# Optimization experiments

Hardware: AMD Instinct MI355X
Metric: run time of the kernel (lower is better)

The kernel has to match this reference:

```python
import jax, jax.numpy as jnp
import numpy as np
from jax import lax

EPS = 1e-5  # BatchNorm eps (inference mode)

def _bn(x, g, b, m, v):
    # inference batchnorm over channel axis 1 of NCHW
    s = g / jnp.sqrt(v + EPS)
    return x * s[None, :, None, None] + (b - m * s)[None, :, None, None]

def _conv1x1(w, x):
    # w: [O, C], x: [B, C, H, W]
    return jnp.einsum('oc,bchw->bohw', w, x)

def setup_inputs() -> dict:
    key = jax.random.key(0)
    ks = jax.random.split(key, 40)
    B, Cin, S = 8, 2048, 64
    R, D, H, NC = 128, 512, 64, 19
    f32 = jnp.float32
    def n(k, shape, scale):
        return jax.random.normal(k, shape, dtype=f32) * scale
    inp = {}
    inp['x'] = jax.random.normal(ks[0], (B, Cin, S, S), f32)
    inp['feat_w'] = n(ks[1], (D, Cin, 3, 3), 0.02)
    # 4 batchnorms: feat, encoding, fusion, conv6
    for i, name in enumerate(['bn1', 'bn2', 'bn3', 'bn4']):
        kk = jax.random.split(ks[2 + i], 4)
        inp[name + '_g'] = jax.random.uniform(kk[0], (D,), f32, 0.5, 1.5)
        inp[name + '_b'] = n(kk[1], (D,), 0.05)
        inp[name + '_m'] = n(kk[2], (D,), 0.1)
        inp[name + '_v'] = jax.random.uniform(kk[3], (D,), f32, 0.5, 1.5)
    inp['enc_w'] = n(ks[6], (D, D), 0.05)
    inp['fc_w'] = n(ks[7], (D, D), 0.05)
    inp['fc_b'] = n(ks[8], (D,), 0.05)
    inp['w1'] = n(ks[9], (R, D, D), 0.05)   # conv1_1[i]: 512->512 1x1
    inp['w2'] = n(ks[10], (R, H, H), 0.05)  # conv1_2[i]: 64->64 1x1
    inp['w3'] = n(ks[11], (R, H, H), 0.05)  # conv1_3[i]: 64->64 1x1
    inp['fusion_w'] = n(ks[12], (D, D), 0.05)
    inp['c6a_w'] = n(ks[13], (D, 2 * D), 0.05)
    inp['c6b_w'] = n(ks[14], (NC, D), 0.05)
    inp['c6b_b'] = n(ks[15], (NC,), 0.05)
    return inp

def reference(x, feat_w,
              bn1_g, bn1_b, bn1_m, bn1_v,
              bn2_g, bn2_b, bn2_m, bn2_v,
              bn3_g, bn3_b, bn3_m, bn3_v,
              bn4_g, bn4_b, bn4_m, bn4_v,
              enc_w, fc_w, fc_b, w1, w2, w3,
              fusion_w, c6a_w, c6b_w, c6b_b):
    # self.feat: 3x3 conv -> BN -> ReLU
    feat = jax.nn.relu(_bn(
        lax.conv_general_dilated(x, feat_w, (1, 1), 'SAME',
                                 dimension_numbers=('NCHW', 'OIHW', 'NCHW')),
        bn1_g, bn1_b, bn1_m, bn1_v))

    # EncModule (se_loss=False)
    enc = jax.nn.relu(_bn(_conv1x1(enc_w, feat), bn2_g, bn2_b, bn2_m, bn2_v))
    en = enc.mean(axis=(2, 3))                                # [B, 512]
    gamma = jax.nn.sigmoid(en @ fc_w.T + fc_b)                # [B, 512]
    se_out = jax.nn.relu(feat * (1.0 + gamma[:, :, None, None]))

    # ContextDecomp: pooled mode vectors (AdaptiveAvgPool2d(1) of permutes)
    Cvec = feat.mean(axis=(2, 3))   # [B, 512] channel vector
    Hvec = feat.mean(axis=(1, 2))   # [B, 64]  (avg over channel & height -> width axis)
    Wvec = feat.mean(axis=(1, 3))   # [B, 64]  (avg over channel & width  -> height axis)
    # all 128 rank-wise 1x1 convs + sigmoid, batched over rank r
    CC = jax.nn.sigmoid(jnp.einsum('roc,bc->bro', w1, Cvec))  # [B, R, 512]
    HH = jax.nn.sigmoid(jnp.einsum('roh,bh->bro', w2, Hvec))  # [B, R, 64]
    WW = jax.nn.sigmoid(jnp.einsum('row,bw->bro', w3, Wvec))  # [B, R, 64]
    # Tucker/CP reconstruction summed over ranks; torch layout puts the
    # width-derived vector (HH) on spatial axis 2 and height-derived (WW) on axis 3
    t1 = jnp.einsum('brc,bri,brj->bcij', CC, HH, WW) * 0.015625  # 1/64
    t = feat * (1.0 + t1)
    outs = jax.nn.relu(_bn(_conv1x1(fusion_w, t), bn3_g, bn3_b, bn3_m, bn3_v))

    # conv6 head: cat -> 1x1 conv -> BN -> ReLU -> (dropout eval=id) -> 1x1 conv
    cat = jnp.concatenate([outs, se_out], axis=1)              # [B, 1024, 64, 64]
    h6 = jax.nn.relu(_bn(_conv1x1(c6a_w, cat), bn4_g, bn4_b, bn4_m, bn4_v))
    out = _conv1x1(c6b_w, h6) + c6b_b[None, :, None, None]     # [B, 19, 64, 64]
    return out
```

## Files before the change

kernel.cpp:

```cpp
#include <hip/hip_runtime.h>
#include <stdint.h>
#include <stddef.h>

using u16 = unsigned short;
using u32 = unsigned int;

typedef __attribute__((ext_vector_type(8))) short short8;
typedef __attribute__((ext_vector_type(4))) float f32x4;

#define DEV static __device__ __forceinline__

DEV float bf2f(u16 v){ union{u32 u; float f;} x; x.u = ((u32)v)<<16; return x.f; }
DEV u16 f2bf(float f){ union{float f; u32 u;} x; x.f = f; u32 r = (x.u + 0x7FFFu + ((x.u>>16)&1u))>>16; return (u16)r; }
DEV float lo16(u32 u){ union{u32 u; float f;} x; x.u = u<<16; return x.f; }
DEV float hi16(u32 u){ union{u32 u; float f;} x; x.u = u & 0xFFFF0000u; return x.f; }

DEV void gload16(const u16* g, u16* l){
  __builtin_amdgcn_global_load_lds((const __attribute__((address_space(1))) void*)g,
                                   (__attribute__((address_space(3))) void*)l, 16, 0, 0);
}

#define BAR    __builtin_amdgcn_s_barrier()
#define SCHED0 __builtin_amdgcn_sched_barrier(0)
#define PRIO1  __builtin_amdgcn_s_setprio(1)
#define PRIO0  __builtin_amdgcn_s_setprio(0)
#define VMC4   asm volatile("s_waitcnt vmcnt(4)" ::: "memory")
#define VMC0   asm volatile("s_waitcnt vmcnt(0)" ::: "memory")

__global__ __launch_bounds__(512, 2)
void conv_gemm256(const u16* __restrict__ xp, const u16* __restrict__ wt,
                  u16* __restrict__ O, const float* __restrict__ sb,
                  float* __restrict__ Cvec, float* __restrict__ Hvec,
                  float* __restrict__ Wvec)
{
  constexpr int NT = 288;
  __shared__ u16 smA[2*256*64];
  __shared__ u16 smB[2*256*64];
  const int t = threadIdx.x;
  const int lane = t & 63;
  const int wv = t >> 6;
  const int wr = wv >> 2, wc = wv & 3;
  const int mt = blockIdx.x, nt = blockIdx.y, b = blockIdx.z;
  const int ij0 = mt*256, n0 = nt*256;
  const u16* Ab = xp + (size_t)b*66*66*2048;

  const int tA   = t >> 3;
  const int sc8  = ((t&7) ^ ((t>>3)&7)) * 8;
  const int ldsc = (t&7) * 8;
  const int qB   = t >> 8;
  const int rB   = (t>>3) & 31;

  f32x4 acc[8][4];
  #pragma unroll
  for (int i=0;i<8;++i)
    #pragma unroll
    for (int j=0;j<4;++j) acc[i][j] = (f32x4){0.f,0.f,0.f,0.f};

  short8 aR[4][2];
  short8 bR[2][2][2];

#define STG_A(dst, s, kt_) do{ \
    const int ktc = (kt_) < NT ? (kt_) : (NT-1); \
    const int tap = ktc>>5; const int ty = (tap*11)>>5; const int tx = tap - ty*3; \
    const size_t ko = ((size_t)(ktc&31))<<6; \
    _Pragma("unroll") for (int l=0;l<2;++l){ \
      const int row = (s)*64 + tA + l*128; \
      const u16* src = Ab + ((size_t)((mt*4 + (s) + l*2 + ty)*66 + tA + tx))*2048 + ko + sc8; \
      gload16(src, (dst) + row*64 + ldsc); } }while(0)

#define STG_B(dst, s, kt_) do{ \
    const int ktc = (kt_) < NT ? (kt_) : (NT-1); \
    const int tap = ktc>>5; \
    const size_t ko = (size_t)tap*2048 + (((size_t)(ktc&31))<<6); \
    _Pragma("unroll") for (int l=0;l<2;++l){ \
      const int row = (l*2 + qB)*64 + (s)*32 + rB; \
      const u16* src = wt + ((size_t)(n0 + row))*9*2048 + ko + sc8; \
      gload16(src, (dst) + row*64 + ldsc); } }while(0)

#define LDA_(base, mh) do{ _Pragma("unroll") for(int mi=0;mi<4;++mi){ \
    const int r = wr*128 + (mh)*64 + mi*16 + (lane&15); \
    _Pragma("unroll") for(int kk=0;kk<2;++kk){ \
      const int ch = (kk*4 + (lane>>4)) ^ (r&7); \
      aR[mi][kk] = *(const short8*)&(base)[r*64 + ch*8]; } } }while(0)
#define LDB_(base, nh) do{ _Pragma("unroll") for(int ni=0;ni<2;++ni){ \
    const int r = wc*64 + (nh)*32 + ni*16 + (lane&15); \
    _Pragma("unroll") for(int kk=0;kk<2;++kk){ \
      const int ch = (kk*4 + (lane>>4)) ^ (r&7); \
      bR[nh][ni][kk] = *(const short8*)&(base)[r*64 + ch*8]; } } }while(0)
#define MFMAQ(mh, nh) do{ _Pragma("unroll") for(int mi=0;mi<4;++mi) \
    _Pragma("unroll") for(int ni=0;ni<2;++ni){ \
      acc[(mh)*4+mi][(nh)*2+ni] = __builtin_amdgcn_mfma_f32_16x16x32_bf16(aR[mi][0], bR[nh][ni][0], acc[(mh)*4+mi][(nh)*2+ni],0,0,0); \
      acc[(mh)*4+mi][(nh)*2+ni] = __builtin_amdgcn_mfma_f32_16x16x32_bf16(aR[mi][1], bR[nh][ni][1], acc[(mh)*4+mi][(nh)*2+ni],0,0,0); } }while(0)

  STG_A(smA, 0, 0);
  STG_B(smB, 0, 0);
  STG_B(smB, 1, 0);
  STG_A(smA, 1, 0);
  VMC4;
  BAR; SCHED0;

  for (int j=0; j<NT; ++j) {
    const int p = j & 1;
    const u16* As = smA + (p<<14);
    const u16* Bs = smB + (p<<14);
    u16* Aalt = smA + ((p^1)<<14);
    u16* Balt = smB + ((p^1)<<14);

    LDA_(As, 0); LDB_(Bs, 0);
    STG_A(Aalt, 0, j+1);
    BAR; SCHED0;
    PRIO1; MFMAQ(0,0); PRIO0;
    VMC4;
    BAR; SCHED0;

    LDB_(Bs, 1);
    STG_B(Balt, 0, j+1);
    BAR; SCHED0;
    PRIO1; MFMAQ(0,1); PRIO0;
    VMC4;
    BAR; SCHED0;

    LDA_(As, 1);
    STG_B(Balt, 1, j+1);
    BAR; SCHED0;
    PRIO1; MFMAQ(1,0); PRIO0;
    BAR; SCHED0;

    STG_A(Aalt, 1, j+1);
    BAR; SCHED0;
    PRIO1; MFMAQ(1,1); PRIO0;
    VMC4;
    BAR; SCHED0;
  }

  VMC0;
  BAR;
  float* red = (float*)smA;
  if (t < 324) red[t] = 0.f;
  BAR;

  float xs[4][4];
  #pragma unroll
  for (int q=0;q<4;++q)
    #pragma unroll
    for (int j2=0;j2<4;++j2) xs[q][j2] = 0.f;
  float ys0 = 0.f, ys1 = 0.f;

  #pragma unroll
  for (int n=0; n<4; ++n) {
    const int cloc = wc*64 + (n>>1)*32 + (n&1)*16 + (lane&15);
    const int col = n0 + cloc;
    const float s = sb[col], bb = sb[512+col];
    float cs = 0.f;
    #pragma unroll
    for (int a=0; a<8; ++a) {
      const int row0 = ij0 + wr*128 + (a>>2)*64 + (a&3)*16 + ((lane>>4)<<2);
      #pragma unroll
      for (int j2=0; j2<4; ++j2) {
        const size_t idx = ((size_t)(b*4096 + row0 + j2))*512 + col;
        float v = acc[a][n][j2]*s + bb;
        v = v > 0.f ? v : 0.f;
        O[idx] = f2bf(v);
        cs += v;
        xs[a&3][j2] += v;
        if (a < 4) ys0 += v; else ys1 += v;
      }
    }
    atomicAdd(&red[cloc], cs);
  }
  #pragma unroll
  for (int off=1; off<16; off<<=1)
    #pragma unroll
    for (int q=0;q<4;++q)
      #pragma unroll
      for (int j2=0;j2<4;++j2) xs[q][j2] += __shfl_xor(xs[q][j2], off);
  if ((lane & 15) == 0) {
    #pragma unroll
    for (int q=0;q<4;++q)
      #pragma unroll
      for (int j2=0;j2<4;++j2)
        atomicAdd(&red[256 + q*16 + (lane>>4)*4 + j2], xs[q][j2]);
  }
  #pragma unroll
  for (int off=1; off<64; off<<=1) { ys0 += __shfl_xor(ys0, off); ys1 += __shfl_xor(ys1, off); }
  if (lane == 0) {
    atomicAdd(&red[320 + wr*2 + 0], ys0);
    atomicAdd(&red[320 + wr*2 + 1], ys1);
  }
  BAR;
  if (t < 256)       atomicAdd(&Cvec[b*512 + n0 + t], red[t]*(1.0f/4096.0f));
  else if (t < 320)  atomicAdd(&Hvec[b*64 + (t-256)], red[t]*(1.0f/32768.0f));
  else if (t < 324)  atomicAdd(&Wvec[b*64 + (ij0>>6) + (t-320)], red[t]*(1.0f/32768.0f));
#undef STG_A
#undef STG_B
#undef LDA_
#undef LDB_
#undef MFMAQ
}

template<int V>
__global__ __launch_bounds__(512, 2)
void gemm256(const u16* __restrict__ A0, const u16* __restrict__ A1,
             const u16* __restrict__ Bw0, const u16* __restrict__ Bw1,
             u16* __restrict__ O, const float* __restrict__ sb,
             float* __restrict__ en)
{
  constexpr int NTALL = (V==4) ? 16 : 8;
  __shared__ u16 smA[2*256*64];
  __shared__ u16 smB[2*256*64];
  const int t = threadIdx.x;
  const int lane = t & 63;
  const int wv = t >> 6;
  const int wr = wv >> 2, wc = wv & 3;
  const int mt = blockIdx.x, nt = blockIdx.y, b = blockIdx.z;
  const int ij0 = mt*256, n0 = nt*256;
  const u16* A0b = A0 + (size_t)b*4096*512;
  const u16* A1b = (V==4) ? (A1 + (size_t)b*4096*512) : nullptr;
  const u16* B1b = (V==4) ? (Bw1 + (size_t)b*512*512) : nullptr;

  const int tA   = t >> 3;
  const int sc8  = ((t&7) ^ ((t>>3)&7)) * 8;
  const int ldsc = (t&7) * 8;
  const int qB   = t >> 8;
  const int rB   = (t>>3) & 31;

  f32x4 acc[8][4];
  #pragma unroll
  for (int i=0;i<8;++i)
    #pragma unroll
    for (int j=0;j<4;++j) acc[i][j] = (f32x4){0.f,0.f,0.f,0.f};

  short8 aR[4][2];
  short8 bR[2][2][2];

#define STG_A(dst, s, kt_) do{ \
    const int ktc = (kt_) < NTALL ? (kt_) : (NTALL-1); \
    const u16* Abase = (V==4 && ktc>=8) ? A1b : A0b; \
    const size_t ko = ((size_t)(ktc&7))<<6; \
    _Pragma("unroll") for (int l=0;l<2;++l){ \
      const int row = (s)*64 + tA + l*128; \
      const u16* src = Abase + (size_t)(ij0 + row)*512 + ko + sc8; \
      gload16(src, (dst) + row*64 + ldsc); } }while(0)

#define STG_B(dst, s, kt_) do{ \
    const int ktc = (kt_) < NTALL ? (kt_) : (NTALL-1); \
    const u16* Bbase = (V==4 && ktc>=8) ? B1b : Bw0; \
    const size_t ko = ((size_t)(ktc&7))<<6; \
    _Pragma("unroll") for (int l=0;l<2;++l){ \
      const int row = (l*2 + qB)*64 + (s)*32 + rB; \
      const u16* src = Bbase + (size_t)(n0 + row)*512 + ko + sc8; \
      gload16(src, (dst) + row*64 + ldsc); } }while(0)

#define LDA_(base, mh) do{ _Pragma("unroll") for(int mi=0;mi<4;++mi){ \
    const int r = wr*128 + (mh)*64 + mi*16 + (lane&15); \
    _Pragma("unroll") for(int kk=0;kk<2;++kk){ \
      const int ch = (kk*4 + (lane>>4)) ^ (r&7); \
      aR[mi][kk] = *(const short8*)&(base)[r*64 + ch*8]; } } }while(0)
#define LDB_(base, nh) do{ _Pragma("unroll") for(int ni=0;ni<2;++ni){ \
    const int r = wc*64 + (nh)*32 + ni*16 + (lane&15); \
    _Pragma("unroll") for(int kk=0;kk<2;++kk){ \
      const int ch = (kk*4 + (lane>>4)) ^ (r&7); \
      bR[nh][ni][kk] = *(const short8*)&(base)[r*64 + ch*8]; } } }while(0)
#define MFMAQ(mh, nh) do{ _Pragma("unroll") for(int mi=0;mi<4;++mi) \
    _Pragma("unroll") for(int ni=0;ni<2;++ni){ \
      acc[(mh)*4+mi][(nh)*2+ni] = __builtin_amdgcn_mfma_f32_16x16x32_bf16(aR[mi][0], bR[nh][ni][0], acc[(mh)*4+mi][(nh)*2+ni],0,0,0); \
      acc[(mh)*4+mi][(nh)*2+ni] = __builtin_amdgcn_mfma_f32_16x16x32_bf16(aR[mi][1], bR[nh][ni][1], acc[(mh)*4+mi][(nh)*2+ni],0,0,0); } }while(0)

  STG_A(smA, 0, 0);
  STG_B(smB, 0, 0);
  STG_B(smB, 1, 0);
  STG_A(smA, 1, 0);
  VMC4;
  BAR; SCHED0;

  for (int j=0; j<NTALL; ++j) {
    const int p = j & 1;
    const u16* As = smA + (p<<14);
    const u16* Bs = smB + (p<<14);
    u16* Aalt = smA + ((p^1)<<14);
    u16* Balt = smB + ((p^1)<<14);

    LDA_(As, 0); LDB_(Bs, 0);
    STG_A(Aalt, 0, j+1);
    BAR; SCHED0;
    PRIO1; MFMAQ(0,0); PRIO0;
    VMC4;
    BAR; SCHED0;

    LDB_(Bs, 1);
    STG_B(Balt, 0, j+1);
    BAR; SCHED0;
    PRIO1; MFMAQ(0,1); PRIO0;
    VMC4;
    BAR; SCHED0;

    LDA_(As, 1);
    STG_B(Balt, 1, j+1);
    BAR; SCHED0;
    PRIO1; MFMAQ(1,0); PRIO0;
    BAR; SCHED0;

    STG_A(Aalt, 1, j+1);
    BAR; SCHED0;
    PRIO1; MFMAQ(1,1); PRIO0;
    VMC4;
    BAR; SCHED0;
  }
  VMC0;

  if constexpr (V==1) {
    #pragma unroll
    for (int n=0; n<4; ++n) {
      const int col = n0 + wc*64 + (n>>1)*32 + (n&1)*16 + (lane&15);
      const float s = sb[col], bb = sb[512+col];
      float cs = 0.f;
      #pragma unroll
      for (int a=0; a<8; ++a) {
        #pragma unroll
        for (int j2=0; j2<4; ++j2) {
          float v = acc[a][n][j2]*s + bb;
          cs += (v > 0.f) ? v : 0.f;
        }
      }
      cs += __shfl_xor(cs, 16);
      cs += __shfl_xor(cs, 32);
      if (lane < 16) atomicAdd(&en[b*512 + col], cs * (1.0f/4096.0f));
    }
  } else {
    #pragma unroll
    for (int n=0; n<4; ++n) {
      const int col = n0 + wc*64 + (n>>1)*32 + (n&1)*16 + (lane&15);
      const float s = sb[col], bb = sb[512+col];
      #pragma unroll
      for (int a=0; a<8; ++a) {
        const int row0 = ij0 + wr*128 + (a>>2)*64 + (a&3)*16 + ((lane>>4)<<2);
        #pragma unroll
        for (int j2=0; j2<4; ++j2) {
          const size_t idx = ((size_t)(b*4096 + row0 + j2))*512 + col;
          float v = acc[a][n][j2]*s + bb;
          O[idx] = f2bf(v > 0.f ? v : 0.f);
        }
      }
    }
  }
#undef STG_A
#undef STG_B
#undef LDA_
#undef LDB_
#undef MFMAQ
}

template<int V>
__global__ __launch_bounds__(256)
void gemm128(const u16* __restrict__ A, const u16* __restrict__ Bw, u16* __restrict__ O,
             const u16* __restrict__ feat, const u16* __restrict__ B2,
             const float* __restrict__ sb, float* __restrict__ en)
{
  constexpr int KSEG = 128;
  __shared__ u16 smA[128*64];
  __shared__ u16 smB[128*64];
  const int tid = threadIdx.x;
  const int lane = tid & 63;
  const int wv = tid >> 6;
  const int wr = wv >> 1, wc = wv & 1;
  const int mt = blockIdx.x, nt = blockIdx.y, b = blockIdx.z;
  const int ij0 = mt*128, n0 = nt*128;
  const int srow = tid >> 3, schunk = tid & 7;

  f32x4 acc[4][4];
  #pragma unroll
  for (int i=0;i<4;++i)
    #pragma unroll
    for (int j=0;j<4;++j) acc[i][j] = (f32x4){0.f,0.f,0.f,0.f};

  const u16* Ab = A + (size_t)b*4096*128;
  const u16* Bb = Bw + (size_t)b*512*128;

  for (int kt=0; kt<KSEG/64; ++kt) {
    const int k0 = kt*64;
    #pragma unroll
    for (int i=0;i<4;++i) {
      const int row = i*32 + srow;
      const int sc = schunk ^ (row & 7);
      gload16(Ab + (size_t)(ij0+row)*128 + (k0 + sc*8), &smA[row*64 + schunk*8]);
    }
    #pragma unroll
    for (int i=0;i<4;++i) {
      const int row = i*32 + srow;
      const int sc = schunk ^ (row & 7);
      gload16(Bb + (size_t)(n0+row)*128 + (k0 + sc*8), &smB[row*64 + schunk*8]);
    }
    __syncthreads();
    #pragma unroll
    for (int ks=0; ks<2; ++ks) {
      short8 av[4], bv[4];
      #pragma unroll
      for (int mi=0;mi<4;++mi) {
        const int r = wr*64 + mi*16 + (lane & 15);
        const int ch = (ks*4 + (lane>>4)) ^ (r & 7);
        av[mi] = *(const short8*)&smA[r*64 + ch*8];
      }
      #pragma unroll
      for (int ni=0;ni<4;++ni) {
        const int r = wc*64 + ni*16 + (lane & 15);
        const int ch = (ks*4 + (lane>>4)) ^ (r & 7);
        bv[ni] = *(const short8*)&smB[r*64 + ch*8];
      }
      #pragma unroll
      for (int mi=0;mi<4;++mi)
        #pragma unroll
        for (int ni=0;ni<4;++ni)
          acc[mi][ni] = __builtin_amdgcn_mfma_f32_16x16x32_bf16(av[mi], bv[ni], acc[mi][ni], 0, 0, 0);
    }
    __syncthreads();
  }

  #pragma unroll
  for (int ni=0;ni<4;++ni) {
    const int col = n0 + wc*64 + ni*16 + (lane & 15);
    #pragma unroll
    for (int mi=0;mi<4;++mi) {
      const int row0 = ij0 + wr*64 + mi*16 + ((lane>>4)<<2);
      #pragma unroll
      for (int j=0;j<4;++j) {
        const size_t idx = ((size_t)(b*4096 + row0 + j))*512 + col;
        O[idx] = f2bf(bf2f(feat[idx]) * (1.0f + acc[mi][ni][j]));
      }
    }
  }
}

__global__ __launch_bounds__(256)
void prep_weights(const float* __restrict__ fw, const float* __restrict__ encw,
                  const float* __restrict__ fusw, const float* __restrict__ c6aw,
                  const float* g1,const float* b1,const float* m1,const float* v1,
                  const float* g2,const float* b2,const float* m2,const float* v2,
                  const float* g3,const float* b3,const float* m3,const float* v3,
                  const float* g4,const float* b4,const float* m4,const float* v4,
                  u16* __restrict__ wt, u16* __restrict__ encb,
                  u16* __restrict__ fusb, u16* __restrict__ c6a1,
                  float* __restrict__ bnsb)
{
  const int bx = blockIdx.x, t = threadIdx.x;
  if (bx < 512) {
    const int o = bx;
    for (int c = t; c < 2048; c += 256) {
      const float* src = fw + ((size_t)o*2048 + c)*9;
      #pragma unroll
      for (int tt=0; tt<9; ++tt)
        wt[((size_t)o*9 + tt)*2048 + c] = f2bf(src[tt]);
    }
  } else if (bx < 1536) {
    const int i = (bx-512)*256 + t;
    encb[i] = f2bf(encw[i]);
  } else if (bx < 2560) {
    const int i = (bx-1536)*256 + t;
    fusb[i] = f2bf(fusw[i]);
  } else if (bx < 3584) {
    const int i = (bx-2560)*256 + t;
    c6a1[i] = f2bf(c6aw[(size_t)(i>>9)*1024 + (i&511)]);
  } else {
    const int c = (bx-3584)*256 + t;
    if (c < 512) {
      const float eps = 1e-5f;
      float s1 = g1[c]*rsqrtf(v1[c]+eps); bnsb[c]      = s1; bnsb[512+c]  = b1[c]-m1[c]*s1;
      float s2 = g2[c]*rsqrtf(v2[c]+eps); bnsb[1024+c] = s2; bnsb[1536+c] = b2[c]-m2[c]*s2;
      float s3 = g3[c]*rsqrtf(v3[c]+eps); bnsb[2048+c] = s3; bnsb[2560+c] = b3[c]-m3[c]*s3;
      float s4 = g4[c]*rsqrtf(v4[c]+eps); bnsb[3072+c] = s4; bnsb[3584+c] = b4[c]-m4[c]*s4;
    }
  }
}

__global__ __launch_bounds__(256)
void pad_x(const float* __restrict__ x, u16* __restrict__ xp)
{
  __shared__ u16 tile[256*66];
  const int bx = blockIdx.x;
  const int cb = bx & 7, y = (bx>>3) & 63, b = bx >> 9;
  const int t = threadIdx.x;
  const int xcol = t & 63, crow = t >> 6;
  for (int it=0; it<64; ++it) {
    const int cl = it*4 + crow;
    tile[cl*66 + xcol] = f2bf(x[(((size_t)b*2048 + cb*256 + cl)*64 + y)*64 + xcol]);
  }
  __syncthreads();
  const size_t rowbase = (size_t)(b*66 + y + 1)*66;
  for (int px=0; px<64; ++px)
    xp[(rowbase + px + 1)*2048 + cb*256 + t] = tile[t*66 + px];
  xp[rowbase*2048 + cb*256 + t] = 0;
  xp[(rowbase + 65)*2048 + cb*256 + t] = 0;
  if (y == 0) {
    const size_t rb = (size_t)(b*66)*66;
    for (int px=0; px<66; ++px) xp[(rb+px)*2048 + cb*256 + t] = 0;
  }
  if (y == 63) {
    const size_t rb = (size_t)(b*66 + 65)*66;
    for (int px=0; px<66; ++px) xp[(rb+px)*2048 + cb*256 + t] = 0;
  }
}

__global__ __launch_bounds__(256)
void small1(const float* __restrict__ en, const float* __restrict__ fcw, const float* __restrict__ fcb,
            const float* __restrict__ w1, const float* __restrict__ Cvec,
            const float* __restrict__ w2, const float* __restrict__ w3,
            const float* __restrict__ Hvec, const float* __restrict__ Wvec,
            float* __restrict__ gamma, u16* __restrict__ CCT,
            float* __restrict__ HH, float* __restrict__ WW)
{
  const int bx = blockIdx.x, t = threadIdx.x;
  if (bx < 8) {
    __shared__ float enl[512];
    const int b = bx;
    for (int c=t;c<512;c+=256) enl[c] = en[b*512+c];
    __syncthreads();
    for (int o=t;o<512;o+=256) {
      float a = fcb[o];
      const float* wr = fcw + (size_t)o*512;
      for (int c=0;c<512;++c) a += enl[c]*wr[c];
      gamma[b*512+o] = 1.0f/(1.0f+__expf(-a));
    }
  } else if (bx < 136) {
    __shared__ float hl[512], wl[512];
    const int r = bx - 8;
    for (int i=t;i<512;i+=256){ hl[i]=Hvec[i]; wl[i]=Wvec[i]; }
    __syncthreads();
    const int i = t & 63, bh = t >> 6;
    for (int bb=bh; bb<8; bb+=4) {
      float sh=0.f, sw=0.f;
      const float* w2r = w2 + ((size_t)r*64 + i)*64;
      const float* w3r = w3 + ((size_t)r*64 + i)*64;
      #pragma unroll 8
      for (int h=0;h<64;++h){ sh += w2r[h]*hl[bb*64+h]; sw += w3r[h]*wl[bb*64+h]; }
      HH[((size_t)bb*128 + r)*64 + i] = 1.0f/(1.0f+__expf(-sh));
      WW[((size_t)bb*128 + r)*64 + i] = 1.0f/(1.0f+__expf(-sw));
    }
  } else {
    __shared__ float cv[4096];
    for (int i=t;i<4096;i+=256) cv[i] = Cvec[i];
    __syncthreads();
    const int p = (bx-136)*4 + (t>>6);
    const int r = p >> 9, o = p & 511;
    const int lane = t & 63;
    float ab[8] = {0,0,0,0,0,0,0,0};
    const float* w1r = w1 + ((size_t)r*512 + o)*512;
    #pragma unroll
    for (int it=0; it<8; ++it) {
      const float wvv = w1r[it*64 + lane];
      #pragma unroll
      for (int bb=0;bb<8;++bb) ab[bb] += wvv * cv[bb*512 + it*64 + lane];
    }
    #pragma unroll
    for (int off=32; off; off>>=1)
      #pragma unroll
      for (int bb=0;bb<8;++bb) ab[bb] += __shfl_xor(ab[bb], off);
    #pragma unroll
    for (int bb=0;bb<8;++bb)
      if (lane == bb)
        CCT[((size_t)bb*512 + o)*128 + r] = f2bf((1.0f/(1.0f+__expf(-ab[bb]))) * 0.015625f);
  }
}

__global__ __launch_bounds__(256)
void small2(const float* __restrict__ c6aw, const float* __restrict__ gamma,
            const float* __restrict__ HH, const float* __restrict__ WW,
            u16* __restrict__ w2b, u16* __restrict__ HWT)
{
  const int bx = blockIdx.x, t = threadIdx.x;
  if (bx < 4096) {
    const int b = bx >> 9, o = bx & 511;
    const float* src = c6aw + (size_t)o*1024 + 512;
    const float* gmv = gamma + b*512;
    u16* dst = w2b + ((size_t)b*512 + o)*512;
    for (int c=t;c<512;c+=256) dst[c] = f2bf(src[c]*(1.0f+gmv[c]));
  } else {
    __shared__ float wwl[64*129];
    __shared__ float hhy[128];
    const int idx = bx - 4096;
    const int b = idx >> 6, y = idx & 63;
    for (int g=t; g<8192; g+=256){ const int r=g>>6, xx=g&63; wwl[xx*129+r] = WW[((size_t)b*128+r)*64+xx]; }
    if (t < 128) hhy[t] = HH[((size_t)b*128 + t)*64 + y];
    __syncthreads();
    const int r2 = (t & 63)*2, xg = t >> 6;
    for (int xx=xg; xx<64; xx+=4) {
      const float v0 = hhy[r2]   * wwl[xx*129 + r2];
      const float v1 = hhy[r2+1] * wwl[xx*129 + r2 + 1];
      const u32 pk = (u32)f2bf(v0) | ((u32)f2bf(v1)<<16);
      *(u32*)&HWT[((size_t)(b*4096 + y*64 + xx))*128 + r2] = pk;
    }
  }
}

__global__ __launch_bounds__(256)
void c6b_head(const u16* __restrict__ h6, const float* __restrict__ w,
              const float* __restrict__ bias, float* __restrict__ out)
{
  const int gid = blockIdx.x*256 + threadIdx.x;
  const int b = gid >> 12, ij = gid & 4095;
  float acc[19];
  #pragma unroll
  for (int o=0;o<19;++o) acc[o] = bias[o];
  const u16* hp = h6 + (size_t)gid*512;
  for (int c0=0;c0<512;c0+=8) {
    const uint4 d = *(const uint4*)(hp + c0);
    const float f0=lo16(d.x),f1=hi16(d.x),f2=lo16(d.y),f3=hi16(d.y),
                f4=lo16(d.z),f5=hi16(d.z),f6=lo16(d.w),f7=hi16(d.w);
    #pragma unroll
    for (int o=0;o<19;++o) {
      const float* wr = w + o*512 + c0;
      acc[o] += f0*wr[0] + f1*wr[1] + f2*wr[2] + f3*wr[3]
              + f4*wr[4] + f5*wr[5] + f6*wr[6] + f7*wr[7];
    }
  }
  #pragma unroll
  for (int o=0;o<19;++o) out[((size_t)(b*19 + o))*4096 + ij] = acc[o];
}

extern "C" void kernel_launch(void* const* d_in, const int* in_sizes, int n_in,
                              void* d_out, int out_size, void* d_ws, size_t ws_size,
                              hipStream_t stream)
{
  (void)in_sizes; (void)n_in; (void)out_size;
  const float* x     = (const float*)d_in[0];
  const float* fw    = (const float*)d_in[1];
  const float* bnp[16];
  for (int i=0;i<16;++i) bnp[i] = (const float*)d_in[2+i];
  const float* enc_w = (const float*)d_in[18];
  const float* fc_w  = (const float*)d_in[19];
  const float* fc_b  = (const float*)d_in[20];
  const float* w1    = (const float*)d_in[21];
  const float* w2    = (const float*)d_in[22];
  const float* w3    = (const float*)d_in[23];
  const float* fus_w = (const float*)d_in[24];
  const float* c6a_w = (const float*)d_in[25];
  const float* c6b_w = (const float*)d_in[26];
  const float* c6b_b = (const float*)d_in[27];

  char* ws = (char*)d_ws;
  constexpr size_t OFF_XP=0, OFF_T=0, OFF_OUTS=33554432ull, OFF_H6=67108864ull,
    OFF_WT=142737408ull, OFF_FEAT=161611776ull, OFF_HWT=195166208ull, OFF_W2B=203554816ull,
    OFF_CCT=207749120ull, OFF_ENCB=208797696ull, OFF_FUSB=209321984ull, OFF_C6A1=209846272ull,
    OFF_HH=210370560ull, OFF_WW=210632704ull, OFF_EN=210894848ull, OFF_CV=210911232ull,
    OFF_HV=210927616ull, OFF_WV=210929664ull, OFF_GAMMA=210931712ull, OFF_BNSB=210948096ull,
    NEEDED=210964480ull;
  if (ws_size < NEEDED) return;

  u16* xp    = (u16*)(ws + OFF_XP);
  u16* tb    = (u16*)(ws + OFF_T);
  u16* outs  = (u16*)(ws + OFF_OUTS);
  u16* h6    = (u16*)(ws + OFF_H6);
  u16* wt    = (u16*)(ws + OFF_WT);
  u16* featb = (u16*)(ws + OFF_FEAT);
  u16* hwt   = (u16*)(ws + OFF_HWT);
  u16* w2b   = (u16*)(ws + OFF_W2B);
  u16* cct   = (u16*)(ws + OFF_CCT);
  u16* encb  = (u16*)(ws + OFF_ENCB);
  u16* fusb  = (u16*)(ws + OFF_FUSB);
  u16* c6a1  = (u16*)(ws + OFF_C6A1);
  float* HH  = (float*)(ws + OFF_HH);
  float* WW  = (float*)(ws + OFF_WW);
  float* en  = (float*)(ws + OFF_EN);
  float* Cv  = (float*)(ws + OFF_CV);
  float* Hv  = (float*)(ws + OFF_HV);
  float* Wv  = (float*)(ws + OFF_WV);
  float* gm  = (float*)(ws + OFF_GAMMA);
  float* bnsb= (float*)(ws + OFF_BNSB);

  hipMemsetAsync(ws + OFF_EN, 0, 36864, stream);

  prep_weights<<<3586,256,0,stream>>>(fw, enc_w, fus_w, c6a_w,
      bnp[0],bnp[1],bnp[2],bnp[3], bnp[4],bnp[5],bnp[6],bnp[7],
      bnp[8],bnp[9],bnp[10],bnp[11], bnp[12],bnp[13],bnp[14],bnp[15],
      wt, encb, fusb, c6a1, bnsb);
  pad_x<<<4096,256,0,stream>>>(x, xp);
  conv_gemm256<<<dim3(16,2,8),512,0,stream>>>(xp, wt, featb, bnsb, Cv, Hv, Wv);
  gemm256<1><<<dim3(16,2,8),512,0,stream>>>(featb, nullptr, encb, nullptr, nullptr, bnsb+1024, en);
  small1<<<16520,256,0,stream>>>(en, fc_w, fc_b, w1, Cv, w2, w3, Hv, Wv, gm, cct, HH, WW);
  small2<<<4608,256,0,stream>>>(c6a_w, gm, HH, WW, w2b, hwt);
  gemm128<2><<<dim3(32,4,8),256,0,stream>>>(hwt, cct, tb, featb, nullptr, nullptr, nullptr);
  gemm256<3><<<dim3(16,2,8),512,0,stream>>>(tb, nullptr, fusb, nullptr, outs, bnsb+2048, nullptr);
  gemm256<4><<<dim3(16,2,8),512,0,stream>>>(outs, featb, c6a1, w2b, h6, bnsb+3072, nullptr);
  c6b_head<<<128,256,0,stream>>>(h6, c6b_w, c6b_b, (float*)d_out);
}
```

Baseline: 953.7 us.

## Restructure conv GEMM main loop with single-barrier schedule and vectorize helper kernels

```diff
diff --git a/kernel.cpp b/kernel.cpp
--- a/kernel.cpp
+++ b/kernel.cpp
@@ -4,6 +4,7 @@
 
 using u16 = unsigned short;
 using u32 = unsigned int;
+using u64 = unsigned long long;
 
 typedef __attribute__((ext_vector_type(8))) short short8;
 typedef __attribute__((ext_vector_type(4))) float f32x4;
@@ -26,8 +27,9 @@
 #define PRIO0  __builtin_amdgcn_s_setprio(0)
 #define VMC4   asm volatile("s_waitcnt vmcnt(4)" ::: "memory")
 #define VMC0   asm volatile("s_waitcnt vmcnt(0)" ::: "memory")
-
-__global__ __launch_bounds__(512, 2)
+#define SGB(m,n) __builtin_amdgcn_sched_group_barrier((m),(n),0)
+
+__global__ __launch_bounds__(512, 1)
 void conv_gemm256(const u16* __restrict__ xp, const u16* __restrict__ wt,
                   u16* __restrict__ O, const float* __restrict__ sb,
                   float* __restrict__ Cvec, float* __restrict__ Hvec,
@@ -56,7 +58,7 @@
     #pragma unroll
     for (int j=0;j<4;++j) acc[i][j] = (f32x4){0.f,0.f,0.f,0.f};
 
-  short8 aR[4][2];
+  short8 aR[2][4][2];
   short8 bR[2][2][2];
 
 #define STG_A(dst, s, kt_) do{ \
@@ -81,7 +83,7 @@
     const int r = wr*128 + (mh)*64 + mi*16 + (lane&15); \
     _Pragma("unroll") for(int kk=0;kk<2;++kk){ \
       const int ch = (kk*4 + (lane>>4)) ^ (r&7); \
-      aR[mi][kk] = *(const short8*)&(base)[r*64 + ch*8]; } } }while(0)
+      aR[mh][mi][kk] = *(const short8*)&(base)[r*64 + ch*8]; } } }while(0)
 #define LDB_(base, nh) do{ _Pragma("unroll") for(int ni=0;ni<2;++ni){ \
     const int r = wc*64 + (nh)*32 + ni*16 + (lane&15); \
     _Pragma("unroll") for(int kk=0;kk<2;++kk){ \
@@ -89,15 +91,15 @@
       bR[nh][ni][kk] = *(const short8*)&(base)[r*64 + ch*8]; } } }while(0)
 #define MFMAQ(mh, nh) do{ _Pragma("unroll") for(int mi=0;mi<4;++mi) \
     _Pragma("unroll") for(int ni=0;ni<2;++ni){ \
-      acc[(mh)*4+mi][(nh)*2+ni] = __builtin_amdgcn_mfma_f32_16x16x32_bf16(aR[mi][0], bR[nh][ni][0], acc[(mh)*4+mi][(nh)*2+ni],0,0,0); \
-      acc[(mh)*4+mi][(nh)*2+ni] = __builtin_amdgcn_mfma_f32_16x16x32_bf16(aR[mi][1], bR[nh][ni][1], acc[(mh)*4+mi][(nh)*2+ni],0,0,0); } }while(0)
+      acc[(mh)*4+mi][(nh)*2+ni] = __builtin_amdgcn_mfma_f32_16x16x32_bf16(aR[mh][mi][0], bR[nh][ni][0], acc[(mh)*4+mi][(nh)*2+ni],0,0,0); \
+      acc[(mh)*4+mi][(nh)*2+ni] = __builtin_amdgcn_mfma_f32_16x16x32_bf16(aR[mh][mi][1], bR[nh][ni][1], acc[(mh)*4+mi][(nh)*2+ni],0,0,0); } }while(0)
 
   STG_A(smA, 0, 0);
   STG_B(smB, 0, 0);
   STG_B(smB, 1, 0);
   STG_A(smA, 1, 0);
-  VMC4;
-  BAR; SCHED0;
+  VMC0;
+  BAR;
 
   for (int j=0; j<NT; ++j) {
     const int p = j & 1;
@@ -106,35 +108,33 @@
     u16* Aalt = smA + ((p^1)<<14);
     u16* Balt = smB + ((p^1)<<14);
 
+    STG_A(Aalt, 0, j+1);
+    STG_B(Balt, 0, j+1);
+    STG_B(Balt, 1, j+1);
+    STG_A(Aalt, 1, j+1);
+
     LDA_(As, 0); LDB_(Bs, 0);
-    STG_A(Aalt, 0, j+1);
-    BAR; SCHED0;
-    PRIO1; MFMAQ(0,0); PRIO0;
-    VMC4;
-    BAR; SCHED0;
-
-    LDB_(Bs, 1);
-    STG_B(Balt, 0, j+1);
-    BAR; SCHED0;
-    PRIO1; MFMAQ(0,1); PRIO0;
-    VMC4;
-    BAR; SCHED0;
-
-    LDA_(As, 1);
-    STG_B(Balt, 1, j+1);
-    BAR; SCHED0;
-    PRIO1; MFMAQ(1,0); PRIO0;
-    BAR; SCHED0;
-
-    STG_A(Aalt, 1, j+1);
-    BAR; SCHED0;
-    PRIO1; MFMAQ(1,1); PRIO0;
-    VMC4;
-    BAR; SCHED0;
-  }
-
-  VMC0;
-  BAR;
+    LDA_(As, 1); LDB_(Bs, 1);
+
+    PRIO1;
+    MFMAQ(0,0);
+    MFMAQ(1,0);
+    MFMAQ(0,1);
+    MFMAQ(1,1);
+    PRIO0;
+
+    SGB(0x10, 8);
+    SGB(0x100, 12);
+    #pragma unroll
+    for (int u=0; u<8; ++u) { SGB(0x8, 2); SGB(0x100, 1); }
+    #pragma unroll
+    for (int u=0; u<4; ++u) { SGB(0x8, 4); SGB(0x100, 1); }
+    SGB(0x8, 32);
+
+    VMC0;
+    BAR;
+  }
+
   float* red = (float*)smA;
   if (t < 324) red[t] = 0.f;
   BAR;
@@ -474,19 +474,21 @@
 __global__ __launch_bounds__(256)
 void pad_x(const float* __restrict__ x, u16* __restrict__ xp)
 {
-  __shared__ u16 tile[256*66];
+  __shared__ u16 tile[256*68];
   const int bx = blockIdx.x;
   const int cb = bx & 7, y = (bx>>3) & 63, b = bx >> 9;
   const int t = threadIdx.x;
-  const int xcol = t & 63, crow = t >> 6;
-  for (int it=0; it<64; ++it) {
-    const int cl = it*4 + crow;
-    tile[cl*66 + xcol] = f2bf(x[(((size_t)b*2048 + cb*256 + cl)*64 + y)*64 + xcol]);
+  const int xg = t & 15, crow = t >> 4;
+  for (int it=0; it<16; ++it) {
+    const int cl = it*16 + crow;
+    const float4 v = *(const float4*)&x[(((size_t)b*2048 + cb*256 + cl)*64 + y)*64 + xg*4];
+    const u64 pk = (u64)f2bf(v.x) | ((u64)f2bf(v.y)<<16) | ((u64)f2bf(v.z)<<32) | ((u64)f2bf(v.w)<<48);
+    *(u64*)&tile[cl*68 + xg*4] = pk;
   }
   __syncthreads();
   const size_t rowbase = (size_t)(b*66 + y + 1)*66;
   for (int px=0; px<64; ++px)
-    xp[(rowbase + px + 1)*2048 + cb*256 + t] = tile[t*66 + px];
+    xp[(rowbase + px + 1)*2048 + cb*256 + t] = tile[t*68 + px];
   xp[rowbase*2048 + cb*256 + t] = 0;
   xp[(rowbase + 65)*2048 + cb*256 + t] = 0;
   if (y == 0) {
@@ -544,10 +546,14 @@
     float ab[8] = {0,0,0,0,0,0,0,0};
     const float* w1r = w1 + ((size_t)r*512 + o)*512;
     #pragma unroll
-    for (int it=0; it<8; ++it) {
-      const float wvv = w1r[it*64 + lane];
-      #pragma unroll
-      for (int bb=0;bb<8;++bb) ab[bb] += wvv * cv[bb*512 + it*64 + lane];
+    for (int it=0; it<2; ++it) {
+      const float4 w4 = *(const float4*)(w1r + it*256 + lane*4);
+      const int c0 = it*256 + lane*4;
+      #pragma unroll
+      for (int bb=0;bb<8;++bb) {
+        const float4 c4 = *(const float4*)&cv[bb*512 + c0];
+        ab[bb] += w4.x*c4.x + w4.y*c4.y + w4.z*c4.z + w4.w*c4.w;
+      }
     }
     #pragma unroll
     for (int off=32; off; off>>=1)
```

Result: slower. 1.032 ms (+8.2%).
